# Kernel optimization log

Hardware: AMD Instinct MI355X
Metric: run time of the kernel (lower is better)

Reference implementation:

```python
import jax, jax.numpy as jnp
import numpy as np

N_NODES = 100000
N_EDGES = 3200000
N_GRAPHS = 512
F_IN = 256
HID = 16
N_CLS = 8


def setup_inputs() -> dict:
    key = jax.random.key(0)
    ks = jax.random.split(key, 6)
    x = jax.random.normal(ks[0], (N_NODES, F_IN), jnp.float32)
    edge_index = jax.random.randint(ks[1], (2, N_EDGES), 0, N_NODES, dtype=jnp.int64)
    batch = jnp.sort(jax.random.randint(ks[2], (N_NODES,), 0, N_GRAPHS, dtype=jnp.int64))
    W1 = jax.random.normal(ks[3], (F_IN, HID), jnp.float32) / np.float32(np.sqrt(F_IN))
    b1 = jnp.zeros((HID,), jnp.float32)
    W2 = jax.random.normal(ks[4], (HID, N_CLS), jnp.float32) / np.float32(np.sqrt(HID))
    b2 = jnp.zeros((N_CLS,), jnp.float32)
    return {"x": x, "edge_index": edge_index, "batch": batch, "num_graphs": N_GRAPHS,
            "W1": W1, "b1": b1, "W2": W2, "b2": b2}


def _gcn_conv(x, src, dst, W, b, n):
    # PyG GCNConv: linear transform, then sym-normalized scatter-add (self-loops
    # already appended to src/dst by caller), bias added after aggregation.
    h = x @ W  # [N, out]
    deg = jax.ops.segment_sum(jnp.ones_like(dst, h.dtype), dst, num_segments=n)
    dinv = jax.lax.rsqrt(jnp.maximum(deg, 1.0))  # deg >= 1 due to self-loops
    norm = dinv[src] * dinv[dst]  # [E+N]
    out = jax.ops.segment_sum(h[src] * norm[:, None], dst, num_segments=n)
    return out + b


def reference(x, edge_index, batch, num_graphs, W1, b1, W2, b2):
    n = x.shape[0]
    loop = jnp.arange(n, dtype=edge_index.dtype)
    src = jnp.concatenate([edge_index[0], loop])
    dst = jnp.concatenate([edge_index[1], loop])
    h = jax.nn.relu(_gcn_conv(x, src, dst, W1, b1, n))
    h = _gcn_conv(h, src, dst, W2, b2, n)
    # global mean pool over graphs
    sums = jax.ops.segment_sum(h, batch, num_segments=num_graphs)
    cnt = jax.ops.segment_sum(jnp.ones((n,), h.dtype), batch, num_segments=num_graphs)
    return sums / jnp.maximum(cnt, 1.0)[:, None]
```

## Files before the change

kernel.cpp:

```cpp
#include <hip/hip_runtime.h>

#define F_IN 256
#define HID 16
#define NCLS 8
#define BSH 9
#define NPB 512
#define MAXBINS 256
#define BCAP 18432u
#define TILE 8192
#define WIN 8
#define GROWS 64
#define APITCH 280

typedef float f4v __attribute__((ext_vector_type(4)));
typedef float f32x4 __attribute__((ext_vector_type(4)));
typedef _Float16 h2v __attribute__((ext_vector_type(2)));
typedef _Float16 f16x4 __attribute__((ext_vector_type(4)));
typedef _Float16 f16x8 __attribute__((ext_vector_type(8)));

__global__ void k_init(unsigned* __restrict__ binCur, int nbins,
                       const float* __restrict__ W1, _Float16* __restrict__ wfrag,
                       float* __restrict__ cg, int g,
                       float* __restrict__ out, int osz) {
    int t = threadIdx.x;
    if (t < nbins) binCur[t] = (unsigned)t * BCAP;
    if (t < 64) {
        int col = t & 15, k0 = (t >> 4) * 8;
#pragma unroll
        for (int kc = 0; kc < 8; ++kc) {
            f16x8 v;
#pragma unroll
            for (int j = 0; j < 8; ++j)
                v[j] = (_Float16)W1[(kc * 32 + k0 + j) * HID + col];
            *(f16x8*)&wfrag[((size_t)t * 8 + kc) * 8] = v;
        }
    }
    for (int i = t; i < g; i += 256) cg[i] = 0.f;
    for (int i = t; i < osz; i += 256) out[i] = 0.f;
}

__global__ void __launch_bounds__(512) k_binA(const int* __restrict__ src,
                                              const int* __restrict__ dst, int e,
                                              unsigned* __restrict__ binCur,
                                              unsigned* __restrict__ binbuf) {
    __shared__ unsigned scnt[MAXBINS], lbase[MAXBINS], gbase[MAXBINS];
    __shared__ unsigned sbuf[TILE];
    __shared__ unsigned char sbin[TILE];
    int t = threadIdx.x;
    if (t < MAXBINS) scnt[t] = 0u;
    __syncthreads();
    int base = blockIdx.x * TILE;
    unsigned ent[16], rank[16];
    int ebin[16];
#pragma unroll
    for (int i = 0; i < 16; ++i) {
        int j = base + t + i * 512;
        ebin[i] = -1;
        if (j < e) {
            int d = __builtin_nontemporal_load(&dst[j]);
            int s = __builtin_nontemporal_load(&src[j]);
            ent[i] = ((unsigned)s << BSH) | ((unsigned)d & (NPB - 1));
            ebin[i] = d >> BSH;
            rank[i] = atomicAdd(&scnt[ebin[i]], 1u);
        }
    }
    __syncthreads();
    if (t == 0) {
        unsigned run = 0;
        for (int b = 0; b < MAXBINS; ++b) { lbase[b] = run; run += scnt[b]; }
    }
    __syncthreads();
    if (t < MAXBINS && scnt[t] > 0u) gbase[t] = atomicAdd(&binCur[t], scnt[t]);
    __syncthreads();
#pragma unroll
    for (int i = 0; i < 16; ++i)
        if (ebin[i] >= 0) {
            unsigned p = lbase[ebin[i]] + rank[i];
            sbuf[p] = ent[i];
            sbin[p] = (unsigned char)ebin[i];
        }
    __syncthreads();
    int total = e - base; if (total > TILE) total = TILE;
    for (int idx = t; idx < total; idx += 512) {
        int b = sbin[idx];
        __builtin_nontemporal_store(sbuf[idx], &binbuf[gbase[b] + ((unsigned)idx - lbase[b])]);
    }
}

__global__ void __launch_bounds__(256) k_binB(const unsigned* __restrict__ binbuf,
                                              const unsigned* __restrict__ binCur,
                                              int n,
                                              unsigned* __restrict__ srcs,
                                              unsigned* __restrict__ off,
                                              unsigned* __restrict__ degc) {
    __shared__ unsigned hist[NPB];
    __shared__ unsigned pref[NPB];
    __shared__ unsigned s1[256];
    int t = threadIdx.x;
    int b = blockIdx.x;
    unsigned base = (unsigned)b * BCAP;
    unsigned end = binCur[b];
    for (int i = t; i < NPB; i += 256) hist[i] = 0u;
    __syncthreads();
    for (unsigned j = base + t; j < end; j += 256)
        atomicAdd(&hist[__builtin_nontemporal_load(&binbuf[j]) & (NPB - 1)], 1u);
    __syncthreads();
    unsigned h0 = hist[2 * t], h1 = hist[2 * t + 1];
    unsigned pair = h0 + h1;
    s1[t] = pair;
    __syncthreads();
    for (int o = 1; o < 256; o <<= 1) {
        unsigned v = (t >= o) ? s1[t - o] : 0u;
        __syncthreads();
        s1[t] += v;
        __syncthreads();
    }
    unsigned exc = s1[t] - pair;
    pref[2 * t] = exc;
    pref[2 * t + 1] = exc + h0;
    __syncthreads();
    int dbase = b << BSH;
    for (int i = t; i < NPB; i += 256) {
        int d = dbase + i;
        if (d < n) { off[d] = base + pref[i]; degc[d] = hist[i]; }
    }
    __syncthreads();
    for (int i = t; i < NPB; i += 256) hist[i] = 0u;
    __syncthreads();
    for (unsigned j = base + t; j < end; j += 256) {
        unsigned v = __builtin_nontemporal_load(&binbuf[j]);
        unsigned dl = v & (NPB - 1);
        unsigned r = atomicAdd(&hist[dl], 1u);
        srcs[base + pref[dl] + r] = v >> BSH;
    }
}

__global__ void __launch_bounds__(256) k_gemm1(const float* __restrict__ x,
                                               const _Float16* __restrict__ wfrag,
                                               const unsigned* __restrict__ degc,
                                               _Float16* __restrict__ t1h, int n) {
    __shared__ _Float16 xs[4][16 * APITCH];
    int t = threadIdx.x;
    int lane = t & 63;
    int wv = t >> 6;
    int col = lane & 15;
    int k0 = (lane >> 4) * 8;
    f16x8 bfrag[8];
#pragma unroll
    for (int kc = 0; kc < 8; ++kc)
        bfrag[kc] = *(const f16x8*)&wfrag[((size_t)lane * 8 + kc) * 8];
    int rbase = blockIdx.x * GROWS;
    int nrows = n - rbase; if (nrows > GROWS) nrows = GROWS;
#pragma unroll
    for (int it = 0; it < GROWS * 64 / 256; ++it) {
        int q = t + it * 256;
        int row = q >> 6, c4 = q & 63;
        if (row < nrows) {
            f4v v = __builtin_nontemporal_load(
                &((const f4v*)(x + (size_t)(rbase + row) * F_IN))[c4]);
            f16x4 hv;
            hv[0] = (_Float16)v[0]; hv[1] = (_Float16)v[1];
            hv[2] = (_Float16)v[2]; hv[3] = (_Float16)v[3];
            *(f16x4*)&xs[row >> 4][(row & 15) * APITCH + c4 * 4] = hv;
        }
    }
    __syncthreads();
    f32x4 acc = {0.f, 0.f, 0.f, 0.f};
    const _Float16* tile = xs[wv];
    int arow = lane & 15;
#pragma unroll
    for (int kc = 0; kc < 8; ++kc) {
        f16x8 afrag = *(const f16x8*)&tile[arow * APITCH + kc * 32 + k0];
        acc = __builtin_amdgcn_mfma_f32_16x16x32_f16(afrag, bfrag[kc], acc, 0, 0, 0);
    }
    int r0 = (lane >> 4) * 4;
#pragma unroll
    for (int reg = 0; reg < 4; ++reg) {
        int grow = rbase + wv * 16 + r0 + reg;
        if (grow < n) {
            float v = acc[reg] * rsqrtf((float)(degc[grow] + 1u));
            t1h[(size_t)grow * HID + col] = (_Float16)v;
        }
    }
}

__global__ void __launch_bounds__(256) k_agg1g2(const unsigned* __restrict__ srcs,
                                                const unsigned* __restrict__ off,
                                                const unsigned* __restrict__ degc,
                                                const uint2* __restrict__ t1q,
                                                const float* __restrict__ b1,
                                                const float* __restrict__ W2,
                                                unsigned* __restrict__ t2h, int n) {
    __shared__ float w2s[HID * NCLS];
    __shared__ float b1s[HID];
    int t = threadIdx.x;
    if (t < HID * NCLS) w2s[t] = W2[t];
    if (t < HID) b1s[t] = b1[t];
    __syncthreads();
    int d = blockIdx.x * 32 + (t >> 3);
    if (d >= n) return;
    int q4 = t & 3;
    int pr = (t >> 2) & 1;
    unsigned p = off[d];
    unsigned c = degc[d];
    float a0 = 0.f, a1 = 0.f, a2 = 0.f, a3 = 0.f;
    union { unsigned u; h2v h; } cv;
    unsigned i = pr;
    for (; i + 6 < c; i += 8) {
        unsigned s0 = srcs[p + i],     s1 = srcs[p + i + 2];
        unsigned s2 = srcs[p + i + 4], s3 = srcs[p + i + 6];
        uint2 w0 = t1q[(size_t)s0 * 4 + q4];
        uint2 w1 = t1q[(size_t)s1 * 4 + q4];
        uint2 w2 = t1q[(size_t)s2 * 4 + q4];
        uint2 w3 = t1q[(size_t)s3 * 4 + q4];
        cv.u = w0.x; a0 += (float)cv.h[0]; a1 += (float)cv.h[1];
        cv.u = w0.y; a2 += (float)cv.h[0]; a3 += (float)cv.h[1];
        cv.u = w1.x; a0 += (float)cv.h[0]; a1 += (float)cv.h[1];
        cv.u = w1.y; a2 += (float)cv.h[0]; a3 += (float)cv.h[1];
        cv.u = w2.x; a0 += (float)cv.h[0]; a1 += (float)cv.h[1];
        cv.u = w2.y; a2 += (float)cv.h[0]; a3 += (float)cv.h[1];
        cv.u = w3.x; a0 += (float)cv.h[0]; a1 += (float)cv.h[1];
        cv.u = w3.y; a2 += (float)cv.h[0]; a3 += (float)cv.h[1];
    }
    for (; i + 2 < c; i += 4) {
        uint2 w0 = t1q[(size_t)srcs[p + i] * 4 + q4];
        uint2 w1 = t1q[(size_t)srcs[p + i + 2] * 4 + q4];
        cv.u = w0.x; a0 += (float)cv.h[0]; a1 += (float)cv.h[1];
        cv.u = w0.y; a2 += (float)cv.h[0]; a3 += (float)cv.h[1];
        cv.u = w1.x; a0 += (float)cv.h[0]; a1 += (float)cv.h[1];
        cv.u = w1.y; a2 += (float)cv.h[0]; a3 += (float)cv.h[1];
    }
    if (i < c) {
        uint2 w = t1q[(size_t)srcs[p + i] * 4 + q4];
        cv.u = w.x; a0 += (float)cv.h[0]; a1 += (float)cv.h[1];
        cv.u = w.y; a2 += (float)cv.h[0]; a3 += (float)cv.h[1];
    }
    a0 += __shfl_xor(a0, 4, 64);
    a1 += __shfl_xor(a1, 4, 64);
    a2 += __shfl_xor(a2, 4, 64);
    a3 += __shfl_xor(a3, 4, 64);
    uint2 sl = t1q[(size_t)d * 4 + q4];
    cv.u = sl.x; a0 += (float)cv.h[0]; a1 += (float)cv.h[1];
    cv.u = sl.y; a2 += (float)cv.h[0]; a3 += (float)cv.h[1];
    float di = rsqrtf((float)(c + 1u));
    float h0 = fmaxf(di * a0 + b1s[4 * q4 + 0], 0.f);
    float h1 = fmaxf(di * a1 + b1s[4 * q4 + 1], 0.f);
    float h2 = fmaxf(di * a2 + b1s[4 * q4 + 2], 0.f);
    float h3 = fmaxf(di * a3 + b1s[4 * q4 + 3], 0.f);
    float o[NCLS];
#pragma unroll
    for (int cc = 0; cc < NCLS; ++cc)
        o[cc] = h0 * w2s[(4 * q4 + 0) * NCLS + cc] + h1 * w2s[(4 * q4 + 1) * NCLS + cc]
              + h2 * w2s[(4 * q4 + 2) * NCLS + cc] + h3 * w2s[(4 * q4 + 3) * NCLS + cc];
#pragma unroll
    for (int m = 1; m < 4; m <<= 1)
#pragma unroll
        for (int cc = 0; cc < NCLS; ++cc)
            o[cc] += __shfl_xor(o[cc], m, 64);
    if (pr == 0) {
        union { unsigned u; h2v h; } pk;
        pk.h[0] = (_Float16)(o[2 * q4] * di);
        pk.h[1] = (_Float16)(o[2 * q4 + 1] * di);
        t2h[(size_t)d * 4 + q4] = pk.u;
    }
}

__global__ void __launch_bounds__(256) k_agg2pool(const unsigned* __restrict__ srcs,
                                                  const unsigned* __restrict__ off,
                                                  const unsigned* __restrict__ degc,
                                                  const uint2* __restrict__ t2q,
                                                  const float* __restrict__ b2,
                                                  const int* __restrict__ batch,
                                                  float* __restrict__ out,
                                                  float* __restrict__ cg, int n) {
    __shared__ float wacc[WIN * NCLS];
    __shared__ float wcnt[WIN];
    __shared__ int gb_s;
    int t = threadIdx.x;
    int bbase = blockIdx.x * 64;
    if (t < WIN * NCLS) wacc[t] = 0.f;
    if (t < WIN) wcnt[t] = 0.f;
    if (t == 0) gb_s = batch[bbase < n ? bbase : (n - 1)];
    __syncthreads();
    int d = bbase + (t >> 2);
    int q2 = t & 1;
    int pr = (t >> 1) & 1;
    if (d < n) {
        unsigned p = off[d];
        unsigned c = degc[d];
        float a0 = 0.f, a1 = 0.f, a2 = 0.f, a3 = 0.f;
        union { unsigned u; h2v h; } cv;
        unsigned i = pr;
        for (; i + 6 < c; i += 8) {
            uint2 w0 = t2q[(size_t)srcs[p + i] * 2 + q2];
            uint2 w1 = t2q[(size_t)srcs[p + i + 2] * 2 + q2];
            uint2 w2 = t2q[(size_t)srcs[p + i + 4] * 2 + q2];
            uint2 w3 = t2q[(size_t)srcs[p + i + 6] * 2 + q2];
            cv.u = w0.x; a0 += (float)cv.h[0]; a1 += (float)cv.h[1];
            cv.u = w0.y; a2 += (float)cv.h[0]; a3 += (float)cv.h[1];
            cv.u = w1.x; a0 += (float)cv.h[0]; a1 += (float)cv.h[1];
            cv.u = w1.y; a2 += (float)cv.h[0]; a3 += (float)cv.h[1];
            cv.u = w2.x; a0 += (float)cv.h[0]; a1 += (float)cv.h[1];
            cv.u = w2.y; a2 += (float)cv.h[0]; a3 += (float)cv.h[1];
            cv.u = w3.x; a0 += (float)cv.h[0]; a1 += (float)cv.h[1];
            cv.u = w3.y; a2 += (float)cv.h[0]; a3 += (float)cv.h[1];
        }
        for (; i + 2 < c; i += 4) {
            uint2 w0 = t2q[(size_t)srcs[p + i] * 2 + q2];
            uint2 w1 = t2q[(size_t)srcs[p + i + 2] * 2 + q2];
            cv.u = w0.x; a0 += (float)cv.h[0]; a1 += (float)cv.h[1];
            cv.u = w0.y; a2 += (float)cv.h[0]; a3 += (float)cv.h[1];
            cv.u = w1.x; a0 += (float)cv.h[0]; a1 += (float)cv.h[1];
            cv.u = w1.y; a2 += (float)cv.h[0]; a3 += (float)cv.h[1];
        }
        if (i < c) {
            uint2 w = t2q[(size_t)srcs[p + i] * 2 + q2];
            cv.u = w.x; a0 += (float)cv.h[0]; a1 += (float)cv.h[1];
            cv.u = w.y; a2 += (float)cv.h[0]; a3 += (float)cv.h[1];
        }
        a0 += __shfl_xor(a0, 2, 64);
        a1 += __shfl_xor(a1, 2, 64);
        a2 += __shfl_xor(a2, 2, 64);
        a3 += __shfl_xor(a3, 2, 64);
        if (pr == 0) {
            uint2 sl = t2q[(size_t)d * 2 + q2];
            cv.u = sl.x; a0 += (float)cv.h[0]; a1 += (float)cv.h[1];
            cv.u = sl.y; a2 += (float)cv.h[0]; a3 += (float)cv.h[1];
            float di = rsqrtf((float)(c + 1u));
            int f0 = 4 * q2;
            float v0 = di * a0 + b2[f0 + 0];
            float v1 = di * a1 + b2[f0 + 1];
            float v2 = di * a2 + b2[f0 + 2];
            float v3 = di * a3 + b2[f0 + 3];
            int g = batch[d];
            int gi = g - gb_s;
            if (gi < WIN) {
                atomicAdd(&wacc[gi * NCLS + f0 + 0], v0);
                atomicAdd(&wacc[gi * NCLS + f0 + 1], v1);
                atomicAdd(&wacc[gi * NCLS + f0 + 2], v2);
                atomicAdd(&wacc[gi * NCLS + f0 + 3], v3);
                if ((t & 3) == 0) atomicAdd(&wcnt[gi], 1.f);
            } else {
                atomicAdd(&out[(size_t)g * NCLS + f0 + 0], v0);
                atomicAdd(&out[(size_t)g * NCLS + f0 + 1], v1);
                atomicAdd(&out[(size_t)g * NCLS + f0 + 2], v2);
                atomicAdd(&out[(size_t)g * NCLS + f0 + 3], v3);
                if ((t & 3) == 0) atomicAdd(&cg[g], 1.f);
            }
        }
    }
    __syncthreads();
    if (t < WIN * NCLS && wcnt[t >> 3] > 0.f)
        atomicAdd(&out[(size_t)(gb_s + (t >> 3)) * NCLS + (t & 7)], wacc[t]);
    if (t < WIN && wcnt[t] > 0.f) atomicAdd(&cg[gb_s + t], wcnt[t]);
}

__global__ void k_div(float* __restrict__ out, const float* __restrict__ cg, int total) {
    int i = blockIdx.x * blockDim.x + threadIdx.x;
    if (i < total) out[i] /= fmaxf(cg[i / NCLS], 1.0f);
}

extern "C" void kernel_launch(void* const* d_in, const int* in_sizes, int n_in,
                              void* d_out, int out_size, void* d_ws, size_t ws_size,
                              hipStream_t stream) {
    const float* x = (const float*)d_in[0];
    const int* ei = (const int*)d_in[1];
    const int* batch = (const int*)d_in[2];
    const float* W1 = (const float*)d_in[4];
    const float* b1 = (const float*)d_in[5];
    const float* W2 = (const float*)d_in[6];
    const float* b2 = (const float*)d_in[7];

    int n = in_sizes[0] / F_IN;
    int e = in_sizes[1] / 2;
    int g = out_size / NCLS;
    const int* src = ei;
    const int* dst = ei + e;
    int nbins = (n + NPB - 1) >> BSH;

    char* w = (char*)d_ws;
    unsigned* binCur = (unsigned*)w; w += (size_t)MAXBINS * 4;
    unsigned* degc   = (unsigned*)w; w += (size_t)n * 4;
    unsigned* off    = (unsigned*)w; w += (size_t)n * 4;
    unsigned* t1h    = (unsigned*)w; w += (size_t)n * 8 * 4;
    unsigned* t2h    = (unsigned*)w; w += (size_t)n * 4 * 4;
    _Float16* wfrag  = (_Float16*)w; w += (size_t)64 * 8 * 8 * 2;
    float* cg        = (float*)w;    w += (size_t)g * 4;
    w = (char*)(((size_t)w + 255) & ~(size_t)255);
    unsigned* binbuf = (unsigned*)w; w += (size_t)nbins * BCAP * 4;
    unsigned* srcs   = (unsigned*)w; w += (size_t)nbins * BCAP * 4;

    k_init<<<1, 256, 0, stream>>>(binCur, nbins, W1, wfrag, cg, g, (float*)d_out, out_size);
    k_binA<<<(e + TILE - 1) / TILE, 512, 0, stream>>>(src, dst, e, binCur, binbuf);
    k_binB<<<nbins, 256, 0, stream>>>(binbuf, binCur, n, srcs, off, degc);
    k_gemm1<<<(n + GROWS - 1) / GROWS, 256, 0, stream>>>(x, wfrag, degc, (_Float16*)t1h, n);
    k_agg1g2<<<(n + 31) / 32, 256, 0, stream>>>(srcs, off, degc, (const uint2*)t1h,
                                                b1, W2, t2h, n);
    k_agg2pool<<<(n + 63) / 64, 256, 0, stream>>>(srcs, off, degc, (const uint2*)t2h,
                                                  b2, batch, (float*)d_out, cg, n);
    k_div<<<(out_size + 255) / 256, 256, 0, stream>>>((float*)d_out, cg, out_size);
}
```

Measured before the change: 179.1 us.

## Split per-bin CSR build into three kernels across four sub-blocks; unroll aggregation loops

The single per-bin counting-sort kernel becomes three kernels. Four blocks per bin compute partial histograms, a per-bin kernel prefix-scans them into offsets and degrees, and four blocks per bin scatter source ids using those per-split offsets. This raises parallelism from about 196 blocks to about 784, which should fill the GPU better, at the cost of two extra launches and a global partial-histogram round trip. Separately, both aggregation kernels gain a 16-edge unrolled loop to keep more gathers in flight, at some cost in registers.

```diff
diff --git a/kernel.cpp b/kernel.cpp
--- a/kernel.cpp
+++ b/kernel.cpp
@@ -11,6 +11,7 @@
 #define WIN 8
 #define GROWS 64
 #define APITCH 280
+#define BSPLIT 4
 
 typedef float f4v __attribute__((ext_vector_type(4)));
 typedef float f32x4 __attribute__((ext_vector_type(4)));
@@ -87,25 +88,41 @@
     }
 }
 
-__global__ void __launch_bounds__(256) k_binB(const unsigned* __restrict__ binbuf,
-                                              const unsigned* __restrict__ binCur,
-                                              int n,
-                                              unsigned* __restrict__ srcs,
-                                              unsigned* __restrict__ off,
-                                              unsigned* __restrict__ degc) {
+__global__ void __launch_bounds__(256) k_binB1(const unsigned* __restrict__ binbuf,
+                                               const unsigned* __restrict__ binCur,
+                                               unsigned* __restrict__ phist) {
     __shared__ unsigned hist[NPB];
+    int t = threadIdx.x;
+    int b = blockIdx.x >> 2, sp = blockIdx.x & 3;
+    unsigned base = (unsigned)b * BCAP;
+    unsigned cnt = binCur[b] - base;
+    unsigned q = cnt / BSPLIT;
+    unsigned j0 = sp * q, j1 = (sp == BSPLIT - 1) ? cnt : j0 + q;
+    for (int i = t; i < NPB; i += 256) hist[i] = 0u;
+    __syncthreads();
+    for (unsigned j = j0 + t; j < j1; j += 256)
+        atomicAdd(&hist[__builtin_nontemporal_load(&binbuf[base + j]) & (NPB - 1)], 1u);
+    __syncthreads();
+    unsigned* ph = phist + ((size_t)b * BSPLIT + sp) * NPB;
+    for (int i = t; i < NPB; i += 256) ph[i] = hist[i];
+}
+
+__global__ void __launch_bounds__(256) k_binB2(unsigned* __restrict__ phist, int n,
+                                               unsigned* __restrict__ off,
+                                               unsigned* __restrict__ degc) {
+    __shared__ unsigned deg[NPB];
     __shared__ unsigned pref[NPB];
     __shared__ unsigned s1[256];
     int t = threadIdx.x;
     int b = blockIdx.x;
-    unsigned base = (unsigned)b * BCAP;
-    unsigned end = binCur[b];
-    for (int i = t; i < NPB; i += 256) hist[i] = 0u;
-    __syncthreads();
-    for (unsigned j = base + t; j < end; j += 256)
-        atomicAdd(&hist[__builtin_nontemporal_load(&binbuf[j]) & (NPB - 1)], 1u);
-    __syncthreads();
-    unsigned h0 = hist[2 * t], h1 = hist[2 * t + 1];
+    unsigned* ph = phist + (size_t)b * BSPLIT * NPB;
+    for (int i = t; i < NPB; i += 256) {
+        unsigned c0 = ph[i], c1 = ph[NPB + i], c2 = ph[2 * NPB + i], c3 = ph[3 * NPB + i];
+        ph[i] = 0u; ph[NPB + i] = c0; ph[2 * NPB + i] = c0 + c1; ph[3 * NPB + i] = c0 + c1 + c2;
+        deg[i] = c0 + c1 + c2 + c3;
+    }
+    __syncthreads();
+    unsigned h0 = deg[2 * t], h1 = deg[2 * t + 1];
     unsigned pair = h0 + h1;
     s1[t] = pair;
     __syncthreads();
@@ -119,19 +136,40 @@
     pref[2 * t] = exc;
     pref[2 * t + 1] = exc + h0;
     __syncthreads();
+    unsigned base = (unsigned)b * BCAP;
     int dbase = b << BSH;
     for (int i = t; i < NPB; i += 256) {
         int d = dbase + i;
-        if (d < n) { off[d] = base + pref[i]; degc[d] = hist[i]; }
-    }
-    __syncthreads();
-    for (int i = t; i < NPB; i += 256) hist[i] = 0u;
-    __syncthreads();
-    for (unsigned j = base + t; j < end; j += 256) {
-        unsigned v = __builtin_nontemporal_load(&binbuf[j]);
+        if (d < n) { off[d] = base + pref[i]; degc[d] = deg[i]; }
+    }
+}
+
+__global__ void __launch_bounds__(256) k_binB3(const unsigned* __restrict__ binbuf,
+                                               const unsigned* __restrict__ binCur,
+                                               const unsigned* __restrict__ phist,
+                                               const unsigned* __restrict__ off,
+                                               int n, unsigned* __restrict__ srcs) {
+    __shared__ unsigned cst[NPB], cur[NPB], offl[NPB];
+    int t = threadIdx.x;
+    int b = blockIdx.x >> 2, sp = blockIdx.x & 3;
+    unsigned base = (unsigned)b * BCAP;
+    unsigned cnt = binCur[b] - base;
+    unsigned q = cnt / BSPLIT;
+    unsigned j0 = sp * q, j1 = (sp == BSPLIT - 1) ? cnt : j0 + q;
+    const unsigned* ph = phist + ((size_t)b * BSPLIT + sp) * NPB;
+    int dbase = b << BSH;
+    for (int i = t; i < NPB; i += 256) {
+        cst[i] = ph[i];
+        cur[i] = 0u;
+        int d = dbase + i;
+        offl[i] = (d < n) ? off[d] : 0u;
+    }
+    __syncthreads();
+    for (unsigned j = j0 + t; j < j1; j += 256) {
+        unsigned v = __builtin_nontemporal_load(&binbuf[base + j]);
         unsigned dl = v & (NPB - 1);
-        unsigned r = atomicAdd(&hist[dl], 1u);
-        srcs[base + pref[dl] + r] = v >> BSH;
+        unsigned r = atomicAdd(&cur[dl], 1u);
+        srcs[offl[dl] + cst[dl] + r] = v >> BSH;
     }
 }
 
@@ -206,6 +244,36 @@
     float a0 = 0.f, a1 = 0.f, a2 = 0.f, a3 = 0.f;
     union { unsigned u; h2v h; } cv;
     unsigned i = pr;
+    for (; i + 14 < c; i += 16) {
+        unsigned s0 = srcs[p + i],      s1 = srcs[p + i + 2];
+        unsigned s2 = srcs[p + i + 4],  s3 = srcs[p + i + 6];
+        unsigned s4 = srcs[p + i + 8],  s5 = srcs[p + i + 10];
+        unsigned s6 = srcs[p + i + 12], s7 = srcs[p + i + 14];
+        uint2 w0 = t1q[(size_t)s0 * 4 + q4];
+        uint2 w1 = t1q[(size_t)s1 * 4 + q4];
+        uint2 w2 = t1q[(size_t)s2 * 4 + q4];
+        uint2 w3 = t1q[(size_t)s3 * 4 + q4];
+        uint2 w4 = t1q[(size_t)s4 * 4 + q4];
+        uint2 w5 = t1q[(size_t)s5 * 4 + q4];
+        uint2 w6 = t1q[(size_t)s6 * 4 + q4];
+        uint2 w7 = t1q[(size_t)s7 * 4 + q4];
+        cv.u = w0.x; a0 += (float)cv.h[0]; a1 += (float)cv.h[1];
+        cv.u = w0.y; a2 += (float)cv.h[0]; a3 += (float)cv.h[1];
+        cv.u = w1.x; a0 += (float)cv.h[0]; a1 += (float)cv.h[1];
+        cv.u = w1.y; a2 += (float)cv.h[0]; a3 += (float)cv.h[1];
+        cv.u = w2.x; a0 += (float)cv.h[0]; a1 += (float)cv.h[1];
+        cv.u = w2.y; a2 += (float)cv.h[0]; a3 += (float)cv.h[1];
+        cv.u = w3.x; a0 += (float)cv.h[0]; a1 += (float)cv.h[1];
+        cv.u = w3.y; a2 += (float)cv.h[0]; a3 += (float)cv.h[1];
+        cv.u = w4.x; a0 += (float)cv.h[0]; a1 += (float)cv.h[1];
+        cv.u = w4.y; a2 += (float)cv.h[0]; a3 += (float)cv.h[1];
+        cv.u = w5.x; a0 += (float)cv.h[0]; a1 += (float)cv.h[1];
+        cv.u = w5.y; a2 += (float)cv.h[0]; a3 += (float)cv.h[1];
+        cv.u = w6.x; a0 += (float)cv.h[0]; a1 += (float)cv.h[1];
+        cv.u = w6.y; a2 += (float)cv.h[0]; a3 += (float)cv.h[1];
+        cv.u = w7.x; a0 += (float)cv.h[0]; a1 += (float)cv.h[1];
+        cv.u = w7.y; a2 += (float)cv.h[0]; a3 += (float)cv.h[1];
+    }
     for (; i + 6 < c; i += 8) {
         unsigned s0 = srcs[p + i],     s1 = srcs[p + i + 2];
         unsigned s2 = srcs[p + i + 4], s3 = srcs[p + i + 6];
@@ -291,6 +359,32 @@
         float a0 = 0.f, a1 = 0.f, a2 = 0.f, a3 = 0.f;
         union { unsigned u; h2v h; } cv;
         unsigned i = pr;
+        for (; i + 14 < c; i += 16) {
+            uint2 w0 = t2q[(size_t)srcs[p + i] * 2 + q2];
+            uint2 w1 = t2q[(size_t)srcs[p + i + 2] * 2 + q2];
+            uint2 w2 = t2q[(size_t)srcs[p + i + 4] * 2 + q2];
+            uint2 w3 = t2q[(size_t)srcs[p + i + 6] * 2 + q2];
+            uint2 w4 = t2q[(size_t)srcs[p + i + 8] * 2 + q2];
+            uint2 w5 = t2q[(size_t)srcs[p + i + 10] * 2 + q2];
+            uint2 w6 = t2q[(size_t)srcs[p + i + 12] * 2 + q2];
+            uint2 w7 = t2q[(size_t)srcs[p + i + 14] * 2 + q2];
+            cv.u = w0.x; a0 += (float)cv.h[0]; a1 += (float)cv.h[1];
+            cv.u = w0.y; a2 += (float)cv.h[0]; a3 += (float)cv.h[1];
+            cv.u = w1.x; a0 += (float)cv.h[0]; a1 += (float)cv.h[1];
+            cv.u = w1.y; a2 += (float)cv.h[0]; a3 += (float)cv.h[1];
+            cv.u = w2.x; a0 += (float)cv.h[0]; a1 += (float)cv.h[1];
+            cv.u = w2.y; a2 += (float)cv.h[0]; a3 += (float)cv.h[1];
+            cv.u = w3.x; a0 += (float)cv.h[0]; a1 += (float)cv.h[1];
+            cv.u = w3.y; a2 += (float)cv.h[0]; a3 += (float)cv.h[1];
+            cv.u = w4.x; a0 += (float)cv.h[0]; a1 += (float)cv.h[1];
+            cv.u = w4.y; a2 += (float)cv.h[0]; a3 += (float)cv.h[1];
+            cv.u = w5.x; a0 += (float)cv.h[0]; a1 += (float)cv.h[1];
+            cv.u = w5.y; a2 += (float)cv.h[0]; a3 += (float)cv.h[1];
+            cv.u = w6.x; a0 += (float)cv.h[0]; a1 += (float)cv.h[1];
+            cv.u = w6.y; a2 += (float)cv.h[0]; a3 += (float)cv.h[1];
+            cv.u = w7.x; a0 += (float)cv.h[0]; a1 += (float)cv.h[1];
+            cv.u = w7.y; a2 += (float)cv.h[0]; a3 += (float)cv.h[1];
+        }
         for (; i + 6 < c; i += 8) {
             uint2 w0 = t2q[(size_t)srcs[p + i] * 2 + q2];
             uint2 w1 = t2q[(size_t)srcs[p + i + 2] * 2 + q2];
@@ -389,10 +483,13 @@
     w = (char*)(((size_t)w + 255) & ~(size_t)255);
     unsigned* binbuf = (unsigned*)w; w += (size_t)nbins * BCAP * 4;
     unsigned* srcs   = (unsigned*)w; w += (size_t)nbins * BCAP * 4;
+    unsigned* phist  = (unsigned*)w; w += (size_t)nbins * BSPLIT * NPB * 4;
 
     k_init<<<1, 256, 0, stream>>>(binCur, nbins, W1, wfrag, cg, g, (float*)d_out, out_size);
     k_binA<<<(e + TILE - 1) / TILE, 512, 0, stream>>>(src, dst, e, binCur, binbuf);
-    k_binB<<<nbins, 256, 0, stream>>>(binbuf, binCur, n, srcs, off, degc);
+    k_binB1<<<nbins * BSPLIT, 256, 0, stream>>>(binbuf, binCur, phist);
+    k_binB2<<<nbins, 256, 0, stream>>>(phist, n, off, degc);
+    k_binB3<<<nbins * BSPLIT, 256, 0, stream>>>(binbuf, binCur, phist, off, n, srcs);
     k_gemm1<<<(n + GROWS - 1) / GROWS, 256, 0, stream>>>(x, wfrag, degc, (_Float16*)t1h, n);
     k_agg1g2<<<(n + 31) / 32, 256, 0, stream>>>(srcs, off, degc, (const uint2*)t1h,
                                                 b1, W2, t2h, n);
```

Result: slower. 186.4 us (+4.1%).
